# Kernel tuning notes

Hardware: AMD Instinct MI355X
Metric: run time of the kernel (lower is better)

Reference implementation:

```python
import jax, jax.numpy as jnp
import numpy as np

K = 10
BN_EPS = 1e-5


def _edgeconv(x, W, b, gamma, beta):
    """DGCNN EdgeConv: kNN on x, edge feat [x_i, x_j - x_i], Linear->(BN)->ReLU, max over k.
    x: [N, C]; W: [2C, Cout]; gamma/beta: [Cout] or None."""
    sq = jnp.sum(x * x, axis=1)                      # [N]
    dist = sq[:, None] + sq[None, :] - 2.0 * (x @ x.T)  # [N, N] squared dists
    _, idx = jax.lax.top_k(-dist, K)                 # [N, K] (includes self)
    xj = x[idx]                                      # [N, K, C] gather
    xi = jnp.broadcast_to(x[:, None, :], xj.shape)   # [N, K, C]
    e = jnp.concatenate([xi, xj - xi], axis=-1)      # [N, K, 2C]
    h = e @ W + b                                    # [N, K, Cout]
    if gamma is not None:                            # BatchNorm1d (training-mode batch stats)
        mu = h.mean(axis=(0, 1))
        var = h.var(axis=(0, 1))
        h = (h - mu) * jax.lax.rsqrt(var + BN_EPS) * gamma + beta
    h = jax.nn.relu(h)
    return h.max(axis=1)                             # [N, Cout]


def _aggregate(f, seg_ids, num_segments):
    return jax.ops.segment_max(f, seg_ids, num_segments=num_segments)


def setup_inputs() -> dict:
    key = jax.random.key(0)
    ks = jax.random.split(key, 12)
    N, B = 16384, 64
    x = jax.random.normal(ks[0], (N, 3), dtype=jnp.float32)
    n_pts = jnp.full((B,), N // B, dtype=jnp.int32)

    def lin(k, fi, fo):
        s = 1.0 / np.sqrt(fi)
        kw, kb = jax.random.split(k)
        return (jax.random.uniform(kw, (fi, fo), jnp.float32, -s, s),
                jax.random.uniform(kb, (fo,), jnp.float32, -s, s))

    W1, b1 = lin(ks[1], 6, 64)
    W2, b2 = lin(ks[2], 128, 64)
    W3, b3 = lin(ks[3], 128, 64)
    W4, b4 = lin(ks[4], 128, 64)
    Wp, bp = lin(ks[5], 256, 128)
    g1 = jnp.ones((64,), jnp.float32); be1 = jnp.zeros((64,), jnp.float32)
    g3 = jnp.ones((64,), jnp.float32); be3 = jnp.zeros((64,), jnp.float32)
    return {"x": x, "n_pts": n_pts,
            "W1": W1, "b1": b1, "g1": g1, "be1": be1,
            "W2": W2, "b2": b2,
            "W3": W3, "b3": b3, "g3": g3, "be3": be3,
            "W4": W4, "b4": b4,
            "Wp": Wp, "bp": bp}


def reference(x, n_pts, W1, b1, g1, be1, W2, b2, W3, b3, g3, be3, W4, b4, Wp, bp):
    N = x.shape[0]
    B = n_pts.shape[0]
    seg_ids = jnp.repeat(jnp.arange(B, dtype=jnp.int32), n_pts, total_repeat_length=N)

    f1 = _edgeconv(x,  W1, b1, g1,  be1)   # [N, 64]
    f2 = _edgeconv(f1, W2, b2, None, None)
    f3 = _edgeconv(f2, W3, b3, g3,  be3)
    f4 = _edgeconv(f3, W4, b4, None, None)

    p = jnp.concatenate([_aggregate(f, seg_ids, B) for f in (f1, f2, f3, f4)], axis=1)  # [B, 256]
    f = jnp.tanh(p @ Wp + bp)              # [B, 128]
    f = f / (jnp.linalg.norm(f, axis=1, keepdims=True) + 1e-9)
    return f
```

## Files before the change

### kernel.cpp

```cpp
#include <hip/hip_runtime.h>
#include <hip/hip_bf16.h>

constexpr int N = 16384;
constexpr int KNN = 10;
constexpr int CF = 64;
constexpr int NS64 = 12;
constexpr int NS3 = 12;

#define FBIG 1e30f

typedef __attribute__((ext_vector_type(8))) __bf16 bfv8;
typedef __attribute__((ext_vector_type(4))) float f32x4;

#define TOPK_INSERT(dval, jval)                                            \
  if ((dval) < bmax) {                                                     \
    float mv = bd[0]; int slot = 0;                                        \
    _Pragma("unroll") for (int s_ = 1; s_ < 10; ++s_)                      \
      if (bd[s_] > mv) { mv = bd[s_]; slot = s_; }                         \
    _Pragma("unroll") for (int s_ = 0; s_ < 10; ++s_)                      \
      if (slot == s_) { bd[s_] = (dval); bi[s_] = (jval); }                \
    bmax = bd[0];                                                          \
    _Pragma("unroll") for (int s_ = 1; s_ < 10; ++s_)                      \
      bmax = fmaxf(bmax, bd[s_]);                                          \
  }

__device__ inline ushort bf16_rne(float x) {
  unsigned u = __float_as_uint(x);
  return (ushort)((u + 0x7FFFu + ((u >> 16) & 1u)) >> 16);
}
__device__ inline float bf16_to_f(ushort h) { return __uint_as_float(((unsigned)h) << 16); }

__global__ __launch_bounds__(256) void pack3_kernel(const float* __restrict__ X,
                                                    float4* __restrict__ xp,
                                                    int* __restrict__ gtauI,
                                                    float* __restrict__ accum) {
  int i = blockIdx.x * 256 + threadIdx.x;
  float x0 = X[3 * i], x1 = X[3 * i + 1], x2 = X[3 * i + 2];
  float s = fmaf(x0, x0, fmaf(x1, x1, x2 * x2));
  xp[i] = make_float4(x0, x1, x2, s);
  gtauI[i] = 0x7F7F7F7F;
  if (blockIdx.x == 0 && threadIdx.x < 128) accum[threadIdx.x] = 0.f;
}

__global__ __launch_bounds__(256) void prep128s_kernel(const float* __restrict__ X,
                                                       ushort* __restrict__ Xp,
                                                       float* __restrict__ sq,
                                                       int* __restrict__ gtauI,
                                                       float* __restrict__ accum) {
  int i = blockIdx.x * 256 + threadIdx.x;
  int n = i >> 4, k4 = (i & 15) << 2;
  float4 v = ((const float4*)X)[i];
  float vv[4] = {v.x, v.y, v.z, v.w};
  ushort h[4], lo[4];
#pragma unroll
  for (int k = 0; k < 4; ++k) {
    h[k] = bf16_rne(vv[k]);
    lo[k] = bf16_rne(vv[k] - bf16_to_f(h[k]));
  }
  ushort* row = Xp + (size_t)n * 128;
  *(ushort4*)(row + k4) = make_ushort4(h[0], h[1], h[2], h[3]);
  *(ushort4*)(row + 64 + k4) = make_ushort4(lo[0], lo[1], lo[2], lo[3]);
  float ps = fmaf(vv[0], vv[0], fmaf(vv[1], vv[1], fmaf(vv[2], vv[2], vv[3] * vv[3])));
#pragma unroll
  for (int m = 1; m < 16; m <<= 1) ps += __shfl_xor(ps, m, 16);
  if ((threadIdx.x & 15) == 0) {
    sq[n] = ps;
    gtauI[n] = 0x7F7F7F7F;
  }
  if (blockIdx.x == 0 && threadIdx.x < 128) accum[threadIdx.x] = 0.f;
}

__global__ __launch_bounds__(256, 3) void knn64w_kernel(const ushort* __restrict__ Xp,
                                                        const float* __restrict__ sq,
                                                        int* __restrict__ gtauI,
                                                        float* __restrict__ dpart,
                                                        ushort* __restrict__ ipart) {
  __shared__ float bufD[4][64 * 33];
  __shared__ ushort bufI[4][64 * 34];
  __shared__ __align__(16) float tauS[4][64];
  __shared__ int cntS[4][64];

  const int tid = threadIdx.x;
  const int w = tid >> 6, l = tid & 63, lp = l & 15, g = l >> 4;
  const int rg = blockIdx.x / NS64, cs = blockIdx.x % NS64;
  const int wbase = rg * 256 + w * 64;
  const int myrow = wbase + l;
  const int c0 = (512 * cs) / NS64, c1 = (512 * (cs + 1)) / NS64;

  tauS[w][l] = FBIG;
  cntS[w][l] = 0;
  __builtin_amdgcn_wave_barrier();

  bfv8 aH1[4], aH2[4], aL1[4], aL2[4];
#pragma unroll
  for (int rt = 0; rt < 4; ++rt) {
    const size_t ao = (size_t)(wbase + rt * 16 + lp) * 128 + g * 8;
    aH1[rt] = *(const bfv8*)&Xp[ao];
    aH2[rt] = *(const bfv8*)&Xp[ao + 32];
    aL1[rt] = *(const bfv8*)&Xp[ao + 64];
    aL2[rt] = *(const bfv8*)&Xp[ao + 96];
  }
  float sqi[16];
#pragma unroll
  for (int rt = 0; rt < 4; ++rt)
#pragma unroll
    for (int r = 0; r < 4; ++r) sqi[rt * 4 + r] = sq[wbase + rt * 16 + g * 4 + r];

  float bd[10]; int bi[10]; float bmax = FBIG; float lastPub = FBIG;
#pragma unroll
  for (int s = 0; s < 10; ++s) { bd[s] = FBIG; bi[s] = 0x7fffffff; }
  int gt = 0x7F7F7F7F;

  for (int t = c0; t < c1; ++t) {
    const int col0 = t * 32 + lp;
    const int col1 = col0 + 16;
    const size_t bo0 = (size_t)col0 * 128 + g * 8;
    bfv8 p0 = *(const bfv8*)&Xp[bo0];
    bfv8 p1 = *(const bfv8*)&Xp[bo0 + 32];
    bfv8 p2 = *(const bfv8*)&Xp[bo0 + 64];
    bfv8 p3 = *(const bfv8*)&Xp[bo0 + 96];
    const size_t bo1 = (size_t)col1 * 128 + g * 8;
    bfv8 q0 = *(const bfv8*)&Xp[bo1];
    bfv8 q1 = *(const bfv8*)&Xp[bo1 + 32];
    bfv8 q2 = *(const bfv8*)&Xp[bo1 + 64];
    bfv8 q3 = *(const bfv8*)&Xp[bo1 + 96];
    float sj0 = sq[col0];
    float sj1 = sq[col1];
    int gtn = gtauI[myrow];

    __builtin_amdgcn_wave_barrier();
    {
      const int c = cntS[w][l];
      if (c) {
        const float* bD = &bufD[w][l * 33];
        const ushort* bI = &bufI[w][l * 34];
#pragma unroll 1
        for (int j = 0; j < c; ++j) {
          float d = bD[j];
          int ii = (int)bI[j];
          TOPK_INSERT(d, ii);
        }
        cntS[w][l] = 0;
      }
      tauS[w][l] = fminf(bmax, __int_as_float(gt));
      if (bmax < lastPub) {
        atomicMin(&gtauI[myrow], __float_as_int(bmax));
        lastPub = bmax;
      }
    }
    __builtin_amdgcn_wave_barrier();
    gt = gtn;

#pragma unroll
    for (int rt = 0; rt < 4; ++rt) {
      f32x4 taur = *(const f32x4*)&tauS[w][rt * 16 + g * 4];
      f32x4 acc0 = {0.f, 0.f, 0.f, 0.f};
      acc0 = __builtin_amdgcn_mfma_f32_16x16x32_bf16(aH1[rt], p0, acc0, 0, 0, 0);
      acc0 = __builtin_amdgcn_mfma_f32_16x16x32_bf16(aH2[rt], p1, acc0, 0, 0, 0);
      acc0 = __builtin_amdgcn_mfma_f32_16x16x32_bf16(aH1[rt], p2, acc0, 0, 0, 0);
      acc0 = __builtin_amdgcn_mfma_f32_16x16x32_bf16(aH2[rt], p3, acc0, 0, 0, 0);
      acc0 = __builtin_amdgcn_mfma_f32_16x16x32_bf16(aL1[rt], p0, acc0, 0, 0, 0);
      acc0 = __builtin_amdgcn_mfma_f32_16x16x32_bf16(aL2[rt], p1, acc0, 0, 0, 0);
      f32x4 acc1 = {0.f, 0.f, 0.f, 0.f};
      acc1 = __builtin_amdgcn_mfma_f32_16x16x32_bf16(aH1[rt], q0, acc1, 0, 0, 0);
      acc1 = __builtin_amdgcn_mfma_f32_16x16x32_bf16(aH2[rt], q1, acc1, 0, 0, 0);
      acc1 = __builtin_amdgcn_mfma_f32_16x16x32_bf16(aH1[rt], q2, acc1, 0, 0, 0);
      acc1 = __builtin_amdgcn_mfma_f32_16x16x32_bf16(aH2[rt], q3, acc1, 0, 0, 0);
      acc1 = __builtin_amdgcn_mfma_f32_16x16x32_bf16(aL1[rt], q0, acc1, 0, 0, 0);
      acc1 = __builtin_amdgcn_mfma_f32_16x16x32_bf16(aL2[rt], q1, acc1, 0, 0, 0);
#pragma unroll
      for (int r = 0; r < 4; ++r) {
        const int rloc = rt * 16 + g * 4 + r;
        float d0 = fmaf(-2.f, acc0[r], sqi[rt * 4 + r] + sj0);
        if (d0 < taur[r]) {
          int pos = atomicAdd(&cntS[w][rloc], 1);
          bufD[w][rloc * 33 + pos] = d0;
          bufI[w][rloc * 34 + pos] = (ushort)col0;
        }
        float d1 = fmaf(-2.f, acc1[r], sqi[rt * 4 + r] + sj1);
        if (d1 < taur[r]) {
          int pos = atomicAdd(&cntS[w][rloc], 1);
          bufD[w][rloc * 33 + pos] = d1;
          bufI[w][rloc * 34 + pos] = (ushort)col1;
        }
      }
    }
  }

  __builtin_amdgcn_wave_barrier();
  {
    const int c = cntS[w][l];
    const float* bD = &bufD[w][l * 33];
    const ushort* bI = &bufI[w][l * 34];
#pragma unroll 1
    for (int j = 0; j < c; ++j) {
      float d = bD[j];
      int ii = (int)bI[j];
      TOPK_INSERT(d, ii);
    }
  }
  float* dp = dpart + ((size_t)cs * N + myrow) * 10;
  ushort* ip = ipart + ((size_t)cs * N + myrow) * 10;
#pragma unroll
  for (int s = 0; s < 10; ++s) { dp[s] = bd[s]; ip[s] = (ushort)bi[s]; }
}

__global__ __launch_bounds__(256, 3) void knn3g_kernel(const float4* __restrict__ xp,
                                                       int* __restrict__ gtauI,
                                                       float* __restrict__ dpart,
                                                       ushort* __restrict__ ipart) {
  __shared__ float bufD[4][64 * 33];
  __shared__ ushort bufI[4][64 * 34];
  __shared__ __align__(16) float tauS[4][64];
  __shared__ int cntS[4][64];

  const int tid = threadIdx.x;
  const int w = tid >> 6, l = tid & 63, lp = l & 15, g = l >> 4;
  const int rg = blockIdx.x / NS3, cs = blockIdx.x % NS3;
  const int wbase = rg * 256 + w * 64;
  const int myrow = wbase + l;
  const int c0 = (512 * cs) / NS3, c1 = (512 * (cs + 1)) / NS3;

  tauS[w][l] = FBIG;
  cntS[w][l] = 0;
  __builtin_amdgcn_wave_barrier();

  float4 rw[16];
#pragma unroll
  for (int rt = 0; rt < 4; ++rt)
#pragma unroll
    for (int r = 0; r < 4; ++r) rw[rt * 4 + r] = xp[wbase + rt * 16 + g * 4 + r];

  float bd[10]; int bi[10]; float bmax = FBIG; float lastPub = FBIG;
#pragma unroll
  for (int s = 0; s < 10; ++s) { bd[s] = FBIG; bi[s] = 0x7fffffff; }
  int gt = 0x7F7F7F7F;

  for (int t = c0; t < c1; ++t) {
    const int col0 = t * 32 + lp;
    const int col1 = col0 + 16;
    const float4 oc0 = xp[col0];
    const float4 oc1 = xp[col1];
    int gtn = gtauI[myrow];

    __builtin_amdgcn_wave_barrier();
    {
      const int c = cntS[w][l];
      if (c) {
        const float* bD = &bufD[w][l * 33];
        const ushort* bI = &bufI[w][l * 34];
#pragma unroll 1
        for (int j = 0; j < c; ++j) {
          float d = bD[j];
          int ii = (int)bI[j];
          TOPK_INSERT(d, ii);
        }
        cntS[w][l] = 0;
      }
      tauS[w][l] = fminf(bmax, __int_as_float(gt));
      if (bmax < lastPub) {
        atomicMin(&gtauI[myrow], __float_as_int(bmax));
        lastPub = bmax;
      }
    }
    __builtin_amdgcn_wave_barrier();
    gt = gtn;

#pragma unroll
    for (int rt = 0; rt < 4; ++rt) {
      f32x4 taur = *(const f32x4*)&tauS[w][rt * 16 + g * 4];
#pragma unroll
      for (int r = 0; r < 4; ++r) {
        const float4 m = rw[rt * 4 + r];
        const int rloc = rt * 16 + g * 4 + r;
        float dot0 = fmaf(m.x, oc0.x, fmaf(m.y, oc0.y, m.z * oc0.z));
        float d0 = fmaf(-2.f, dot0, m.w + oc0.w);
        if (d0 < taur[r]) {
          int pos = atomicAdd(&cntS[w][rloc], 1);
          bufD[w][rloc * 33 + pos] = d0;
          bufI[w][rloc * 34 + pos] = (ushort)col0;
        }
        float dot1 = fmaf(m.x, oc1.x, fmaf(m.y, oc1.y, m.z * oc1.z));
        float d1 = fmaf(-2.f, dot1, m.w + oc1.w);
        if (d1 < taur[r]) {
          int pos = atomicAdd(&cntS[w][rloc], 1);
          bufD[w][rloc * 33 + pos] = d1;
          bufI[w][rloc * 34 + pos] = (ushort)col1;
        }
      }
    }
  }

  __builtin_amdgcn_wave_barrier();
  {
    const int c = cntS[w][l];
    const float* bD = &bufD[w][l * 33];
    const ushort* bI = &bufI[w][l * 34];
#pragma unroll 1
    for (int j = 0; j < c; ++j) {
      float d = bD[j];
      int ii = (int)bI[j];
      TOPK_INSERT(d, ii);
    }
  }
  float* dp = dpart + ((size_t)cs * N + myrow) * 10;
  ushort* ip = ipart + ((size_t)cs * N + myrow) * 10;
#pragma unroll
  for (int s = 0; s < 10; ++s) { dp[s] = bd[s]; ip[s] = (ushort)bi[s]; }
}

template <int S>
__global__ __launch_bounds__(256) void merge_kernel(const float* __restrict__ dpart,
                                                    const ushort* __restrict__ ipart,
                                                    ushort* __restrict__ idx_out) {
  const int row = blockIdx.x * 256 + threadIdx.x;
  float d[S * 10]; int id_[S * 10];
#pragma unroll
  for (int p = 0; p < S; ++p)
#pragma unroll
    for (int s = 0; s < 10; ++s) {
      d[p * 10 + s] = dpart[((size_t)p * N + row) * 10 + s];
      id_[p * 10 + s] = (int)ipart[((size_t)p * N + row) * 10 + s];
    }
#pragma unroll
  for (int t = 0; t < 10; ++t) {
    float dm = d[0]; int im = id_[0]; int slot = 0;
#pragma unroll
    for (int e = 1; e < S * 10; ++e) {
      bool better = (d[e] < dm) || (d[e] == dm && id_[e] < im);
      if (better) { dm = d[e]; im = id_[e]; slot = e; }
    }
    idx_out[(size_t)row * 10 + t] = (ushort)im;
#pragma unroll
    for (int e = 0; e < S * 10; ++e)
      if (e == slot) d[e] = FBIG;
  }
}

__global__ __launch_bounds__(256) void uv_kernel(const float* __restrict__ Xf, int CIN,
                                                 const float* __restrict__ W,
                                                 const float* __restrict__ bias,
                                                 float* __restrict__ U, float* __restrict__ V) {
  __shared__ float Ws[8192];
  int tid = threadIdx.x;
  int c = tid & 63, p = tid >> 6;
  int n = blockIdx.x * 4 + p;
  const int tot = CIN * 128;
  for (int i = tid; i < tot; i += 256) Ws[i] = W[i];
  __syncthreads();
  const float* xr = Xf + (size_t)n * CIN;
  float vt = 0.f, vb = 0.f;
  for (int m = 0; m < CIN; ++m) {
    float xm = xr[m];
    vt = fmaf(xm, Ws[m * 64 + c], vt);
    vb = fmaf(xm, Ws[(CIN + m) * 64 + c], vb);
  }
  U[(size_t)n * 64 + c] = vb;
  V[(size_t)n * 64 + c] = vt - vb + bias[c];
}

__global__ __launch_bounds__(256) void stats_kernel(const float* __restrict__ U,
                                                    const float* __restrict__ V,
                                                    const ushort* __restrict__ idx,
                                                    float* __restrict__ accum) {
  int tid = threadIdx.x;
  int c = tid & 63, p = tid >> 6;
  int base = blockIdx.x * 64;
  float s = 0.f, s2 = 0.f;
  for (int ch = 0; ch < 16; ++ch) {
    int n = base + ch * 4 + p;
    float vn = V[(size_t)n * 64 + c];
    const ushort* in_ = idx + (size_t)n * 10;
#pragma unroll
    for (int k = 0; k < 10; ++k) {
      float h = vn + U[(size_t)in_[k] * 64 + c];
      s += h;
      s2 = fmaf(h, h, s2);
    }
  }
  __shared__ float red[256], red2[256];
  red[tid] = s; red2[tid] = s2;
  __syncthreads();
  if (tid < 64) {
    float ts = red[tid] + red[64 + tid] + red[128 + tid] + red[192 + tid];
    float t2 = red2[tid] + red2[64 + tid] + red2[128 + tid] + red2[192 + tid];
    atomicAdd(&accum[tid], ts);
    atomicAdd(&accum[64 + tid], t2);
  }
}

__global__ void bnfin_kernel(const float* __restrict__ accum,
                             const float* __restrict__ gamma,
                             const float* __restrict__ beta,
                             float* __restrict__ scale, float* __restrict__ shift) {
  int c = threadIdx.x;
  float inv = 1.f / (float)(N * KNN);
  float mu = accum[c] * inv;
  float var = accum[64 + c] * inv - mu * mu;
  float sc = gamma[c] * rsqrtf(var + 1e-5f);
  scale[c] = sc;
  shift[c] = fmaf(-mu, sc, beta[c]);
}

__global__ __launch_bounds__(256) void apply_kernel(const float* __restrict__ U,
                                                    const float* __restrict__ V,
                                                    const ushort* __restrict__ idx,
                                                    const float* __restrict__ scale,
                                                    const float* __restrict__ shift,
                                                    int use_bn, float* __restrict__ Fout) {
  int tid = threadIdx.x;
  int c = tid & 63, p = tid >> 6;
  int n = blockIdx.x * 4 + p;
  float sc = use_bn ? scale[c] : 1.f;
  float sh = use_bn ? shift[c] : 0.f;
  float vn = V[(size_t)n * 64 + c];
  const ushort* in_ = idx + (size_t)n * 10;
  float m = 0.f;
#pragma unroll
  for (int k = 0; k < 10; ++k) {
    float h = vn + U[(size_t)in_[k] * 64 + c];
    m = fmaxf(m, fmaf(h, sc, sh));
  }
  Fout[(size_t)n * 64 + c] = m;
}

__global__ __launch_bounds__(256) void pool1_kernel(const float* __restrict__ f1,
                                                    const float* __restrict__ f2,
                                                    const float* __restrict__ f3,
                                                    const float* __restrict__ f4,
                                                    const int* __restrict__ n_pts,
                                                    float* __restrict__ Pp) {
  int b = blockIdx.x >> 2;
  int q = blockIdx.x & 3;
  int c = threadIdx.x;
  int off = 0;
  for (int i = 0; i < b; ++i) off += n_pts[i];
  int cnt_ = n_pts[b];
  int s0 = off + (cnt_ * q) / 4;
  int s1 = off + (cnt_ * (q + 1)) / 4;
  const float* f = (c < 64) ? f1 : (c < 128) ? f2 : (c < 192) ? f3 : f4;
  int ch = c & 63;
  float m = -3.4e38f;
  for (int t = s0; t < s1; ++t) m = fmaxf(m, f[(size_t)t * 64 + ch]);
  Pp[((size_t)q * 64 + b) * 256 + c] = m;
}

__global__ __launch_bounds__(128) void head_kernel(const float* __restrict__ Pp,
                                                   const float* __restrict__ Wp,
                                                   const float* __restrict__ bp,
                                                   float* __restrict__ out) {
  int b = blockIdx.x;
  int c = threadIdx.x;
  __shared__ float ps[256];
#pragma unroll
  for (int j = 0; j < 2; ++j) {
    int cc = c + j * 128;
    float m = Pp[(size_t)b * 256 + cc];
#pragma unroll
    for (int q = 1; q < 4; ++q) m = fmaxf(m, Pp[((size_t)q * 64 + b) * 256 + cc]);
    ps[cc] = m;
  }
  __syncthreads();
  float acc = bp[c];
  for (int m = 0; m < 256; ++m) acc = fmaf(ps[m], Wp[m * 128 + c], acc);
  float t = tanhf(acc);
  __shared__ float red[128];
  red[c] = t * t;
  __syncthreads();
  for (int s = 64; s > 0; s >>= 1) {
    if (c < s) red[c] += red[c + s];
    __syncthreads();
  }
  float nrm = sqrtf(red[0]);
  out[b * 128 + c] = t / (nrm + 1e-9f);
}

extern "C" void kernel_launch(void* const* d_in, const int* in_sizes, int n_in,
                              void* d_out, int out_size, void* d_ws, size_t ws_size,
                              hipStream_t stream) {
  const float* x = (const float*)d_in[0];
  const int* n_pts = (const int*)d_in[1];
  const float* W1 = (const float*)d_in[2];
  const float* b1 = (const float*)d_in[3];
  const float* g1 = (const float*)d_in[4];
  const float* be1 = (const float*)d_in[5];
  const float* W2 = (const float*)d_in[6];
  const float* b2 = (const float*)d_in[7];
  const float* W3 = (const float*)d_in[8];
  const float* b3 = (const float*)d_in[9];
  const float* g3 = (const float*)d_in[10];
  const float* be3 = (const float*)d_in[11];
  const float* W4 = (const float*)d_in[12];
  const float* b4 = (const float*)d_in[13];
  const float* Wp = (const float*)d_in[14];
  const float* bp = (const float*)d_in[15];
  float* out = (float*)d_out;

  char* w = (char*)d_ws;
  auto alloc = [&](size_t bytes) {
    char* p = w;
    w += (bytes + 255) & ~(size_t)255;
    return p;
  };
  const size_t FS = (size_t)N * 64 * 4;
  float* f1 = (float*)alloc(FS);
  float* f2 = (float*)alloc(FS);
  float* f3 = (float*)alloc(FS);
  float* f4 = (float*)alloc(FS);
  float* Ub = (float*)alloc(FS);
  float* dpartf = (float*)alloc((size_t)NS64 * N * 10 * 4);
  ushort* iparti = (ushort*)alloc((size_t)NS64 * N * 10 * 2);
  float4* xp = (float4*)alloc((size_t)N * 16);
  float* sqb = (float*)alloc((size_t)N * 4);
  int* gtauI = (int*)alloc((size_t)N * 4);
  ushort* idxb = (ushort*)alloc((size_t)N * 10 * 2);
  float* accum = (float*)alloc(512);
  float* scaleb = (float*)alloc(256);
  float* shiftb = (float*)alloc(256);
  float* Ppart = (float*)alloc((size_t)4 * 64 * 256 * 4);
  ushort* Xp128 = (ushort*)Ub;
  float* Vb = dpartf;
  (void)ws_size; (void)n_in; (void)in_sizes; (void)out_size;

  auto run_layer = [&](const float* fin, int cin, const float* W, const float* b,
                       const float* g, const float* be, int use_bn, float* fout) {
    if (cin == 3) {
      pack3_kernel<<<N / 256, 256, 0, stream>>>(fin, xp, gtauI, accum);
      knn3g_kernel<<<64 * NS3, 256, 0, stream>>>(xp, gtauI, dpartf, iparti);
      merge_kernel<NS3><<<N / 256, 256, 0, stream>>>(dpartf, iparti, idxb);
    } else {
      prep128s_kernel<<<N * 64 / 4 / 256, 256, 0, stream>>>(fin, Xp128, sqb, gtauI, accum);
      knn64w_kernel<<<64 * NS64, 256, 0, stream>>>(Xp128, sqb, gtauI, dpartf, iparti);
      merge_kernel<NS64><<<N / 256, 256, 0, stream>>>(dpartf, iparti, idxb);
    }
    uv_kernel<<<N / 4, 256, 0, stream>>>(fin, cin, W, b, Ub, Vb);
    if (use_bn) {
      stats_kernel<<<256, 256, 0, stream>>>(Ub, Vb, idxb, accum);
      bnfin_kernel<<<1, 64, 0, stream>>>(accum, g, be, scaleb, shiftb);
    }
    apply_kernel<<<N / 4, 256, 0, stream>>>(Ub, Vb, idxb, scaleb, shiftb, use_bn, fout);
  };

  run_layer(x, 3, W1, b1, g1, be1, 1, f1);
  run_layer(f1, 64, W2, b2, nullptr, nullptr, 0, f2);
  run_layer(f2, 64, W3, b3, g3, be3, 1, f3);
  run_layer(f3, 64, W4, b4, nullptr, nullptr, 0, f4);
  pool1_kernel<<<256, 256, 0, stream>>>(f1, f2, f3, f4, n_pts, Ppart);
  head_kernel<<<64, 128, 0, stream>>>(Ppart, Wp, bp, out);
}
```

Measured before the change: 1.222 ms.

## Halve kNN candidate buffers, drain per half-tile, raise occupancy and splits

Shrinks the per-row shared candidate buffers from 33 to 17 slots and adds a drain step between the two 16-column halves of each tile so the smaller buffers cannot overflow. The smaller LDS footprint lets the kNN kernels target four blocks per CU, and the column split count rises from 12 to 16. The merge kernel is rewritten as a streaming top-10 insertion over partitions instead of holding all S*10 candidates in registers, and now launches 64-thread blocks. The extra drain and barriers add per-tile overhead, and the larger split count writes more partial results for the merge to read.

Result: slower. 3.252 ms (+166.0%).

```diff
diff --git a/kernel.cpp b/kernel.cpp
--- a/kernel.cpp
+++ b/kernel.cpp
@@ -4,8 +4,8 @@
 constexpr int N = 16384;
 constexpr int KNN = 10;
 constexpr int CF = 64;
-constexpr int NS64 = 12;
-constexpr int NS3 = 12;
+constexpr int NS64 = 16;
+constexpr int NS3 = 16;
 
 #define FBIG 1e30f
 
@@ -70,13 +70,13 @@
   if (blockIdx.x == 0 && threadIdx.x < 128) accum[threadIdx.x] = 0.f;
 }
 
-__global__ __launch_bounds__(256, 3) void knn64w_kernel(const ushort* __restrict__ Xp,
+__global__ __launch_bounds__(256, 4) void knn64w_kernel(const ushort* __restrict__ Xp,
                                                         const float* __restrict__ sq,
                                                         int* __restrict__ gtauI,
                                                         float* __restrict__ dpart,
                                                         ushort* __restrict__ ipart) {
-  __shared__ float bufD[4][64 * 33];
-  __shared__ ushort bufI[4][64 * 34];
+  __shared__ float bufD[4][64 * 17];
+  __shared__ ushort bufI[4][64 * 18];
   __shared__ __align__(16) float tauS[4][64];
   __shared__ int cntS[4][64];
 
@@ -110,6 +110,22 @@
 #pragma unroll
   for (int s = 0; s < 10; ++s) { bd[s] = FBIG; bi[s] = 0x7fffffff; }
   int gt = 0x7F7F7F7F;
+
+#define DRAIN_KNN64()                                                      \
+  {                                                                        \
+    const int c_ = cntS[w][l];                                             \
+    if (c_) {                                                              \
+      const float* bD = &bufD[w][l * 17];                                  \
+      const ushort* bI = &bufI[w][l * 18];                                 \
+      _Pragma("unroll 1") for (int j = 0; j < c_; ++j) {                   \
+        float d = bD[j];                                                   \
+        int ii = (int)bI[j];                                               \
+        TOPK_INSERT(d, ii);                                                \
+      }                                                                    \
+      cntS[w][l] = 0;                                                      \
+    }                                                                      \
+    tauS[w][l] = fminf(bmax, __int_as_float(gt));                          \
+  }
 
   for (int t = c0; t < c1; ++t) {
     const int col0 = t * 32 + lp;
@@ -129,24 +145,10 @@
     int gtn = gtauI[myrow];
 
     __builtin_amdgcn_wave_barrier();
-    {
-      const int c = cntS[w][l];
-      if (c) {
-        const float* bD = &bufD[w][l * 33];
-        const ushort* bI = &bufI[w][l * 34];
-#pragma unroll 1
-        for (int j = 0; j < c; ++j) {
-          float d = bD[j];
-          int ii = (int)bI[j];
-          TOPK_INSERT(d, ii);
-        }
-        cntS[w][l] = 0;
-      }
-      tauS[w][l] = fminf(bmax, __int_as_float(gt));
-      if (bmax < lastPub) {
-        atomicMin(&gtauI[myrow], __float_as_int(bmax));
-        lastPub = bmax;
-      }
+    DRAIN_KNN64();
+    if (bmax < lastPub) {
+      atomicMin(&gtauI[myrow], __float_as_int(bmax));
+      lastPub = bmax;
     }
     __builtin_amdgcn_wave_barrier();
     gt = gtn;
@@ -161,6 +163,25 @@
       acc0 = __builtin_amdgcn_mfma_f32_16x16x32_bf16(aH2[rt], p3, acc0, 0, 0, 0);
       acc0 = __builtin_amdgcn_mfma_f32_16x16x32_bf16(aL1[rt], p0, acc0, 0, 0, 0);
       acc0 = __builtin_amdgcn_mfma_f32_16x16x32_bf16(aL2[rt], p1, acc0, 0, 0, 0);
+#pragma unroll
+      for (int r = 0; r < 4; ++r) {
+        const int rloc = rt * 16 + g * 4 + r;
+        float d0 = fmaf(-2.f, acc0[r], sqi[rt * 4 + r] + sj0);
+        if (d0 < taur[r]) {
+          int pos = atomicAdd(&cntS[w][rloc], 1);
+          bufD[w][rloc * 17 + pos] = d0;
+          bufI[w][rloc * 18 + pos] = (ushort)col0;
+        }
+      }
+    }
+
+    __builtin_amdgcn_wave_barrier();
+    DRAIN_KNN64();
+    __builtin_amdgcn_wave_barrier();
+
+#pragma unroll
+    for (int rt = 0; rt < 4; ++rt) {
+      f32x4 taur = *(const f32x4*)&tauS[w][rt * 16 + g * 4];
       f32x4 acc1 = {0.f, 0.f, 0.f, 0.f};
       acc1 = __builtin_amdgcn_mfma_f32_16x16x32_bf16(aH1[rt], q0, acc1, 0, 0, 0);
       acc1 = __builtin_amdgcn_mfma_f32_16x16x32_bf16(aH2[rt], q1, acc1, 0, 0, 0);
@@ -171,46 +192,31 @@
 #pragma unroll
       for (int r = 0; r < 4; ++r) {
         const int rloc = rt * 16 + g * 4 + r;
-        float d0 = fmaf(-2.f, acc0[r], sqi[rt * 4 + r] + sj0);
-        if (d0 < taur[r]) {
-          int pos = atomicAdd(&cntS[w][rloc], 1);
-          bufD[w][rloc * 33 + pos] = d0;
-          bufI[w][rloc * 34 + pos] = (ushort)col0;
-        }
         float d1 = fmaf(-2.f, acc1[r], sqi[rt * 4 + r] + sj1);
         if (d1 < taur[r]) {
           int pos = atomicAdd(&cntS[w][rloc], 1);
-          bufD[w][rloc * 33 + pos] = d1;
-          bufI[w][rloc * 34 + pos] = (ushort)col1;
+          bufD[w][rloc * 17 + pos] = d1;
+          bufI[w][rloc * 18 + pos] = (ushort)col1;
         }
       }
     }
   }
 
   __builtin_amdgcn_wave_barrier();
-  {
-    const int c = cntS[w][l];
-    const float* bD = &bufD[w][l * 33];
-    const ushort* bI = &bufI[w][l * 34];
-#pragma unroll 1
-    for (int j = 0; j < c; ++j) {
-      float d = bD[j];
-      int ii = (int)bI[j];
-      TOPK_INSERT(d, ii);
-    }
-  }
+  DRAIN_KNN64();
+#undef DRAIN_KNN64
   float* dp = dpart + ((size_t)cs * N + myrow) * 10;
   ushort* ip = ipart + ((size_t)cs * N + myrow) * 10;
 #pragma unroll
   for (int s = 0; s < 10; ++s) { dp[s] = bd[s]; ip[s] = (ushort)bi[s]; }
 }
 
-__global__ __launch_bounds__(256, 3) void knn3g_kernel(const float4* __restrict__ xp,
+__global__ __launch_bounds__(256, 4) void knn3g_kernel(const float4* __restrict__ xp,
                                                        int* __restrict__ gtauI,
                                                        float* __restrict__ dpart,
                                                        ushort* __restrict__ ipart) {
-  __shared__ float bufD[4][64 * 33];
-  __shared__ ushort bufI[4][64 * 34];
+  __shared__ float bufD[4][64 * 17];
+  __shared__ ushort bufI[4][64 * 18];
   __shared__ __align__(16) float tauS[4][64];
   __shared__ int cntS[4][64];
 
@@ -236,6 +242,22 @@
   for (int s = 0; s < 10; ++s) { bd[s] = FBIG; bi[s] = 0x7fffffff; }
   int gt = 0x7F7F7F7F;
 
+#define DRAIN_KNN3()                                                       \
+  {                                                                        \
+    const int c_ = cntS[w][l];                                             \
+    if (c_) {                                                              \
+      const float* bD = &bufD[w][l * 17];                                  \
+      const ushort* bI = &bufI[w][l * 18];                                 \
+      _Pragma("unroll 1") for (int j = 0; j < c_; ++j) {                   \
+        float d = bD[j];                                                   \
+        int ii = (int)bI[j];                                               \
+        TOPK_INSERT(d, ii);                                                \
+      }                                                                    \
+      cntS[w][l] = 0;                                                      \
+    }                                                                      \
+    tauS[w][l] = fminf(bmax, __int_as_float(gt));                          \
+  }
+
   for (int t = c0; t < c1; ++t) {
     const int col0 = t * 32 + lp;
     const int col1 = col0 + 16;
@@ -244,24 +266,10 @@
     int gtn = gtauI[myrow];
 
     __builtin_amdgcn_wave_barrier();
-    {
-      const int c = cntS[w][l];
-      if (c) {
-        const float* bD = &bufD[w][l * 33];
-        const ushort* bI = &bufI[w][l * 34];
-#pragma unroll 1
-        for (int j = 0; j < c; ++j) {
-          float d = bD[j];
-          int ii = (int)bI[j];
-          TOPK_INSERT(d, ii);
-        }
-        cntS[w][l] = 0;
-      }
-      tauS[w][l] = fminf(bmax, __int_as_float(gt));
-      if (bmax < lastPub) {
-        atomicMin(&gtauI[myrow], __float_as_int(bmax));
-        lastPub = bmax;
-      }
+    DRAIN_KNN3();
+    if (bmax < lastPub) {
+      atomicMin(&gtauI[myrow], __float_as_int(bmax));
+      lastPub = bmax;
     }
     __builtin_amdgcn_wave_barrier();
     gt = gtn;
@@ -277,32 +285,37 @@
         float d0 = fmaf(-2.f, dot0, m.w + oc0.w);
         if (d0 < taur[r]) {
           int pos = atomicAdd(&cntS[w][rloc], 1);
-          bufD[w][rloc * 33 + pos] = d0;
-          bufI[w][rloc * 34 + pos] = (ushort)col0;
+          bufD[w][rloc * 17 + pos] = d0;
+          bufI[w][rloc * 18 + pos] = (ushort)col0;
         }
+      }
+    }
+
+    __builtin_amdgcn_wave_barrier();
+    DRAIN_KNN3();
+    __builtin_amdgcn_wave_barrier();
+
+#pragma unroll
+    for (int rt = 0; rt < 4; ++rt) {
+      f32x4 taur = *(const f32x4*)&tauS[w][rt * 16 + g * 4];
+#pragma unroll
+      for (int r = 0; r < 4; ++r) {
+        const float4 m = rw[rt * 4 + r];
+        const int rloc = rt * 16 + g * 4 + r;
         float dot1 = fmaf(m.x, oc1.x, fmaf(m.y, oc1.y, m.z * oc1.z));
         float d1 = fmaf(-2.f, dot1, m.w + oc1.w);
         if (d1 < taur[r]) {
           int pos = atomicAdd(&cntS[w][rloc], 1);
-          bufD[w][rloc * 33 + pos] = d1;
-          bufI[w][rloc * 34 + pos] = (ushort)col1;
+          bufD[w][rloc * 17 + pos] = d1;
+          bufI[w][rloc * 18 + pos] = (ushort)col1;
         }
       }
     }
   }
 
   __builtin_amdgcn_wave_barrier();
-  {
-    const int c = cntS[w][l];
-    const float* bD = &bufD[w][l * 33];
-    const ushort* bI = &bufI[w][l * 34];
-#pragma unroll 1
-    for (int j = 0; j < c; ++j) {
-      float d = bD[j];
-      int ii = (int)bI[j];
-      TOPK_INSERT(d, ii);
-    }
-  }
+  DRAIN_KNN3();
+#undef DRAIN_KNN3
   float* dp = dpart + ((size_t)cs * N + myrow) * 10;
   ushort* ip = ipart + ((size_t)cs * N + myrow) * 10;
 #pragma unroll
@@ -310,31 +323,42 @@
 }
 
 template <int S>
-__global__ __launch_bounds__(256) void merge_kernel(const float* __restrict__ dpart,
-                                                    const ushort* __restrict__ ipart,
-                                                    ushort* __restrict__ idx_out) {
-  const int row = blockIdx.x * 256 + threadIdx.x;
-  float d[S * 10]; int id_[S * 10];
-#pragma unroll
-  for (int p = 0; p < S; ++p)
+__global__ __launch_bounds__(64) void merge_kernel(const float* __restrict__ dpart,
+                                                   const ushort* __restrict__ ipart,
+                                                   ushort* __restrict__ idx_out) {
+  const int row = blockIdx.x * 64 + threadIdx.x;
+  float bd[10]; int bi[10];
+#pragma unroll
+  for (int s = 0; s < 10; ++s) { bd[s] = FBIG; bi[s] = 0x7fffffff; }
+  float bmax = FBIG; int bmaxi = 0x7fffffff;
+#pragma unroll 1
+  for (int p = 0; p < S; ++p) {
+    const float* dp = dpart + ((size_t)p * N + row) * 10;
+    const ushort* ip = ipart + ((size_t)p * N + row) * 10;
 #pragma unroll
     for (int s = 0; s < 10; ++s) {
-      d[p * 10 + s] = dpart[((size_t)p * N + row) * 10 + s];
-      id_[p * 10 + s] = (int)ipart[((size_t)p * N + row) * 10 + s];
-    }
-#pragma unroll
-  for (int t = 0; t < 10; ++t) {
-    float dm = d[0]; int im = id_[0]; int slot = 0;
-#pragma unroll
-    for (int e = 1; e < S * 10; ++e) {
-      bool better = (d[e] < dm) || (d[e] == dm && id_[e] < im);
-      if (better) { dm = d[e]; im = id_[e]; slot = e; }
-    }
-    idx_out[(size_t)row * 10 + t] = (ushort)im;
-#pragma unroll
-    for (int e = 0; e < S * 10; ++e)
-      if (e == slot) d[e] = FBIG;
-  }
+      float d = dp[s]; int ii = (int)ip[s];
+      if (d < bmax || (d == bmax && ii < bmaxi)) {
+        int slot = 0; float mv = bd[0]; int mi = bi[0];
+#pragma unroll
+        for (int e = 1; e < 10; ++e) {
+          bool gtr = (bd[e] > mv) || (bd[e] == mv && bi[e] > mi);
+          if (gtr) { mv = bd[e]; mi = bi[e]; slot = e; }
+        }
+#pragma unroll
+        for (int e = 0; e < 10; ++e)
+          if (e == slot) { bd[e] = d; bi[e] = ii; }
+        bmax = bd[0]; bmaxi = bi[0];
+#pragma unroll
+        for (int e = 1; e < 10; ++e) {
+          bool gtr = (bd[e] > bmax) || (bd[e] == bmax && bi[e] > bmaxi);
+          if (gtr) { bmax = bd[e]; bmaxi = bi[e]; }
+        }
+      }
+    }
+  }
+#pragma unroll
+  for (int t = 0; t < 10; ++t) idx_out[(size_t)row * 10 + t] = (ushort)bi[t];
 }
 
 __global__ __launch_bounds__(256) void uv_kernel(const float* __restrict__ Xf, int CIN,
@@ -527,11 +551,11 @@
     if (cin == 3) {
       pack3_kernel<<<N / 256, 256, 0, stream>>>(fin, xp, gtauI, accum);
       knn3g_kernel<<<64 * NS3, 256, 0, stream>>>(xp, gtauI, dpartf, iparti);
-      merge_kernel<NS3><<<N / 256, 256, 0, stream>>>(dpartf, iparti, idxb);
+      merge_kernel<NS3><<<N / 64, 64, 0, stream>>>(dpartf, iparti, idxb);
     } else {
       prep128s_kernel<<<N * 64 / 4 / 256, 256, 0, stream>>>(fin, Xp128, sqb, gtauI, accum);
       knn64w_kernel<<<64 * NS64, 256, 0, stream>>>(Xp128, sqb, gtauI, dpartf, iparti);
-      merge_kernel<NS64><<<N / 256, 256, 0, stream>>>(dpartf, iparti, idxb);
+      merge_kernel<NS64><<<N / 64, 64, 0, stream>>>(dpartf, iparti, idxb);
     }
     uv_kernel<<<N / 4, 256, 0, stream>>>(fin, cin, W, b, Ub, Vb);
     if (use_bn) {
```
